# Kernel optimization log

Hardware: AMD Instinct MI355X
Metric: run time of the kernel (lower is better)

## Reference

```python
import jax, jax.numpy as jnp
import numpy as np

B, H, IN = 2048, 256, 64
K_TERMS = 8


def setup_inputs() -> dict:
    key = jax.random.key(0)
    ks = jax.random.split(key, 8)
    limit_x = float(np.sqrt(6.0 / (IN + H)))
    limit_h = float(np.sqrt(6.0 / (H + H)))
    return {
        "h": jax.random.normal(ks[0], (B, H), dtype=jnp.float32),
        "x": jax.random.normal(ks[1], (B, IN), dtype=jnp.float32),
        "xdot": jax.random.normal(ks[2], (B, IN), dtype=jnp.float32),
        "wx": jax.random.uniform(ks[3], (H, IN), minval=-limit_x, maxval=limit_x, dtype=jnp.float32),
        "wh": jax.random.uniform(ks[4], (H, H), minval=-limit_h, maxval=limit_h, dtype=jnp.float32),
        "wout": jax.random.uniform(ks[5], (H, H), minval=-limit_h, maxval=limit_h, dtype=jnp.float32),
        "b0": jnp.zeros((H,), dtype=jnp.float32),
        "b1": jnp.zeros((H,), dtype=jnp.float32),
    }


def reference(h, x, xdot, wx, wh, wout, b0, b1):
    # Batched version of the per-sample vector field (original is vmapped by the solver).
    l1 = x @ wx.T + h @ wh.T + b0                 # [B,H]
    relu_val = jax.nn.relu(l1)
    lout = relu_val @ wout.T + b1                 # [B,H]
    tanh_val = jnp.tanh(lout)
    dtanh = 1.0 - tanh_val ** 2                   # [B,H]
    drelu = (l1 > 0).astype(jnp.float32)          # activation == 'relu' (hard gate)
    # d_outer[b,i,j] = dtanh[b,i] * wout[i,j] * drelu[b,j]
    d_outer = dtanh[:, :, None] * wout[None, :, :] * drelu[:, None, :]  # [B,H,H]
    Jx = jnp.einsum('bhj,ji->bhi', d_outer, wx)   # [B,H,IN]
    Jh = jnp.einsum('bhj,ji->bhi', d_outer, wh)   # [B,H,H]
    jx = jnp.einsum('bhi,bi->bh', Jx, xdot)       # [B,H]
    h_dot = jx
    curr_term = jx
    for _ in range(K_TERMS):
        curr_term = jnp.einsum('bij,bj->bi', Jh, curr_term)
        h_dot = h_dot + curr_term
    return h_dot
```

## Files before the change

kernel.cpp:

```cpp
#include <hip/hip_runtime.h>
#include <math.h>

#define B_  2048
#define H_  256
#define IN_ 64

typedef __attribute__((ext_vector_type(8))) short bf8_t;
typedef __attribute__((ext_vector_type(4))) short s4_t;
typedef __attribute__((ext_vector_type(4))) float f4_t;

#define MFMA_BF16(a, b, c) __builtin_amdgcn_mfma_f32_16x16x32_bf16((a), (b), (c), 0, 0, 0)

__device__ __forceinline__ short f2bf(float f) {
  union { float f; unsigned u; } v; v.f = f;
  unsigned u = v.u + 0x7fffu + ((v.u >> 16) & 1u);
  return (short)(u >> 16);
}
__device__ __forceinline__ float bf2f(short s) {
  union { unsigned u; float f; } v; v.u = ((unsigned)(unsigned short)s) << 16;
  return v.f;
}

__device__ __forceinline__ void load_wfrag2(const float* __restrict__ W, int ld, int col,
                                            int k0, bf8_t& hi, bf8_t& lo) {
  const float* p = W + (size_t)col * ld + k0;
  f4_t a = *reinterpret_cast<const f4_t*>(p);
  f4_t b = *reinterpret_cast<const f4_t*>(p + 4);
#pragma unroll
  for (int j = 0; j < 8; ++j) {
    float f = (j < 4) ? a[j] : b[j - 4];
    short h = f2bf(f);
    hi[j] = h;
    lo[j] = f2bf(f - bf2f(h));
  }
}

#define GEMM3(A0, A1, AH, AL, WH, WL, NK) do {                                  \
  _Pragma("unroll")                                                             \
  for (int ks = 0; ks < (NK); ++ks) {                                           \
    bf8_t ah = *reinterpret_cast<const bf8_t*>(&AH[ln][ks * 32 + lq * 8]);      \
    bf8_t al = *reinterpret_cast<const bf8_t*>(&AL[ln][ks * 32 + lq * 8]);      \
    A0 = MFMA_BF16(ah, WH[0][ks], A0);                                          \
    A0 = MFMA_BF16(ah, WL[0][ks], A0);                                          \
    A0 = MFMA_BF16(al, WH[0][ks], A0);                                          \
    A1 = MFMA_BF16(ah, WH[1][ks], A1);                                          \
    A1 = MFMA_BF16(ah, WL[1][ks], A1);                                          \
    A1 = MFMA_BF16(al, WH[1][ks], A1);                                          \
  } } while (0)

#define GEMM2(A0, A1, AH, AL, WH, NK) do {                                      \
  _Pragma("unroll")                                                             \
  for (int ks = 0; ks < (NK); ++ks) {                                           \
    bf8_t ah = *reinterpret_cast<const bf8_t*>(&AH[ln][ks * 32 + lq * 8]);      \
    bf8_t al = *reinterpret_cast<const bf8_t*>(&AL[ln][ks * 32 + lq * 8]);      \
    A0 = MFMA_BF16(ah, WH[0][ks], A0);                                          \
    A0 = MFMA_BF16(al, WH[0][ks], A0);                                          \
    A1 = MFMA_BF16(ah, WH[1][ks], A1);                                          \
    A1 = MFMA_BF16(al, WH[1][ks], A1);                                          \
  } } while (0)

__global__ __launch_bounds__(512, 2) void jacde_mfma(
    const float* __restrict__ h_g, const float* __restrict__ x_g,
    const float* __restrict__ xd_g, const float* __restrict__ wx,
    const float* __restrict__ wh, const float* __restrict__ wo,
    const float* __restrict__ b0, const float* __restrict__ b1,
    float* __restrict__ out) {

  __shared__ short h_hi[16][264], h_lo[16][264];
  __shared__ short x_hi[16][72],  x_lo[16][72];
  __shared__ short xd_hi[16][72], xd_lo[16][72];
  __shared__ short u_hi[16][264], u_lo[16][264];
  __shared__ short v_hi[16][264], v_lo[16][264];
  __shared__ float l1_t[16][264];
  __shared__ int   fix_cnt;
  __shared__ int   fix_list[64];

  const int tid  = threadIdx.x;
  const int wv   = tid >> 6;
  const int lane = tid & 63;
  const int ln   = lane & 15;
  const int lq   = lane >> 4;
  const int r0   = blockIdx.x * 16;
  const int cbase = wv * 32;

  if (tid == 0) fix_cnt = 0;

  for (int c = tid; c < 16 * 64; c += 512) {
    int r = c >> 6, k4 = (c & 63) * 4;
    f4_t v = *reinterpret_cast<const f4_t*>(h_g + (size_t)(r0 + r) * H_ + k4);
    s4_t shv, slv;
#pragma unroll
    for (int j = 0; j < 4; ++j) { short h = f2bf(v[j]); shv[j] = h; slv[j] = f2bf(v[j] - bf2f(h)); }
    *reinterpret_cast<s4_t*>(&h_hi[r][k4]) = shv;
    *reinterpret_cast<s4_t*>(&h_lo[r][k4]) = slv;
  }
  {
    int t2 = tid & 255;
    const float* src = (tid < 256) ? x_g : xd_g;
    short (*dh)[72] = (tid < 256) ? x_hi : xd_hi;
    short (*dl)[72] = (tid < 256) ? x_lo : xd_lo;
    int r = t2 >> 4, k4 = (t2 & 15) * 4;
    f4_t v = *reinterpret_cast<const f4_t*>(src + (size_t)(r0 + r) * IN_ + k4);
    s4_t shv, slv;
#pragma unroll
    for (int j = 0; j < 4; ++j) { short h = f2bf(v[j]); shv[j] = h; slv[j] = f2bf(v[j] - bf2f(h)); }
    *reinterpret_cast<s4_t*>(&dh[r][k4]) = shv;
    *reinterpret_cast<s4_t*>(&dl[r][k4]) = slv;
  }

  bf8_t whf[2][8], wof[2][8];
  f4_t acc0, acc1, sacc0, sacc1;
  float dre0[4], dre1[4], dta0[4], dta1[4], hd0[4], hd1[4];

  {
    bf8_t whl[2][8], wxh[2][2], wxl[2][2];
#pragma unroll
    for (int t = 0; t < 2; ++t) {
      int col = cbase + t * 16 + ln;
#pragma unroll
      for (int ks = 0; ks < 8; ++ks)
        load_wfrag2(wh, H_, col, ks * 32 + lq * 8, whf[t][ks], whl[t][ks]);
#pragma unroll
      for (int ks = 0; ks < 2; ++ks)
        load_wfrag2(wx, IN_, col, ks * 32 + lq * 8, wxh[t][ks], wxl[t][ks]);
    }
    __syncthreads();

    float bv0 = b0[cbase + ln], bv1 = b0[cbase + 16 + ln];
    acc0 = (f4_t){bv0, bv0, bv0, bv0};
    acc1 = (f4_t){bv1, bv1, bv1, bv1};
    GEMM3(acc0, acc1, h_hi, h_lo, whf, whl, 8);
    GEMM3(acc0, acc1, x_hi, x_lo, wxh, wxl, 2);
    sacc0 = (f4_t){0.f, 0.f, 0.f, 0.f};
    sacc1 = (f4_t){0.f, 0.f, 0.f, 0.f};
    GEMM3(sacc0, sacc1, xd_hi, xd_lo, wxh, wxl, 2);
#pragma unroll
    for (int r = 0; r < 4; ++r) {
      l1_t[lq * 4 + r][cbase + ln]      = acc0[r];
      l1_t[lq * 4 + r][cbase + 16 + ln] = acc1[r];
    }
  }
  __syncthreads();

  for (int e = tid; e < 16 * 256; e += 512) {
    int r = e >> 8, c = e & 255;
    if (fabsf(l1_t[r][c]) < 1e-4f) {
      int idx = atomicAdd(&fix_cnt, 1);
      if (idx < 64) fix_list[idx] = (r << 8) | c;
    }
  }
  __syncthreads();
  {
    int nfix = min(fix_cnt, 64);
    for (int e = wv; e < nfix; e += 8) {
      int rc = fix_list[e];
      int r = rc >> 8, c = rc & 255;
      const float* hrow = h_g + (size_t)(r0 + r) * H_;
      const float* wrow = wh + (size_t)c * H_;
      double sum = (double)hrow[lane]       * (double)wrow[lane]
                 + (double)hrow[lane + 64]  * (double)wrow[lane + 64]
                 + (double)hrow[lane + 128] * (double)wrow[lane + 128]
                 + (double)hrow[lane + 192] * (double)wrow[lane + 192]
                 + (double)x_g[(size_t)(r0 + r) * IN_ + lane] * (double)wx[(size_t)c * IN_ + lane];
#pragma unroll
      for (int m = 32; m; m >>= 1) sum += __shfl_xor(sum, m);
      if (lane == 0) l1_t[r][c] = (float)(sum + (double)b0[c]);
    }
  }
  __syncthreads();

  for (int e = tid; e < 16 * 256; e += 512) {
    int r = e >> 8, c = e & 255;
    float l1 = l1_t[r][c];
    float rv = l1 > 0.f ? l1 : 0.f;
    short hi = f2bf(rv);
    u_hi[r][c] = hi;
    u_lo[r][c] = f2bf(rv - bf2f(hi));
  }
#pragma unroll
  for (int r = 0; r < 4; ++r) {
    dre0[r] = (l1_t[lq * 4 + r][cbase + ln]      > 0.f) ? 1.f : 0.f;
    dre1[r] = (l1_t[lq * 4 + r][cbase + 16 + ln] > 0.f) ? 1.f : 0.f;
  }
  __syncthreads();

  {
    bf8_t wol[2][8];
#pragma unroll
    for (int t = 0; t < 2; ++t) {
      int col = cbase + t * 16 + ln;
#pragma unroll
      for (int ks = 0; ks < 8; ++ks)
        load_wfrag2(wo, H_, col, ks * 32 + lq * 8, wof[t][ks], wol[t][ks]);
    }
    float bv0 = b1[cbase + ln], bv1 = b1[cbase + 16 + ln];
    acc0 = (f4_t){bv0, bv0, bv0, bv0};
    acc1 = (f4_t){bv1, bv1, bv1, bv1};
    GEMM3(acc0, acc1, u_hi, u_lo, wof, wol, 8);
#pragma unroll
    for (int r = 0; r < 4; ++r) {
      float t0 = tanhf(acc0[r]);
      float t1 = tanhf(acc1[r]);
      dta0[r] = 1.f - t0 * t0;
      dta1[r] = 1.f - t1 * t1;
    }
  }
  __syncthreads();

#pragma unroll
  for (int r = 0; r < 4; ++r) {
    int row = lq * 4 + r;
    float v0 = dre0[r] * sacc0[r];
    float v1 = dre1[r] * sacc1[r];
    short h0 = f2bf(v0), h1 = f2bf(v1);
    u_hi[row][cbase + ln]      = h0;  u_lo[row][cbase + ln]      = f2bf(v0 - bf2f(h0));
    u_hi[row][cbase + 16 + ln] = h1;  u_lo[row][cbase + 16 + ln] = f2bf(v1 - bf2f(h1));
  }
  __syncthreads();

  acc0 = (f4_t){0.f, 0.f, 0.f, 0.f};
  acc1 = (f4_t){0.f, 0.f, 0.f, 0.f};
  GEMM2(acc0, acc1, u_hi, u_lo, wof, 8);
#pragma unroll
  for (int r = 0; r < 4; ++r) {
    int row = lq * 4 + r;
    float v0 = dta0[r] * acc0[r];
    float v1 = dta1[r] * acc1[r];
    hd0[r] = v0; hd1[r] = v1;
    short h0 = f2bf(v0), h1 = f2bf(v1);
    v_hi[row][cbase + ln]      = h0;  v_lo[row][cbase + ln]      = f2bf(v0 - bf2f(h0));
    v_hi[row][cbase + 16 + ln] = h1;  v_lo[row][cbase + 16 + ln] = f2bf(v1 - bf2f(h1));
  }
  __syncthreads();

  for (int it = 0; it < 8; ++it) {
    acc0 = (f4_t){0.f, 0.f, 0.f, 0.f};
    acc1 = (f4_t){0.f, 0.f, 0.f, 0.f};
    GEMM2(acc0, acc1, v_hi, v_lo, whf, 8);
#pragma unroll
    for (int r = 0; r < 4; ++r) {
      int row = lq * 4 + r;
      float v0 = dre0[r] * acc0[r];
      float v1 = dre1[r] * acc1[r];
      short h0 = f2bf(v0), h1 = f2bf(v1);
      u_hi[row][cbase + ln]      = h0;  u_lo[row][cbase + ln]      = f2bf(v0 - bf2f(h0));
      u_hi[row][cbase + 16 + ln] = h1;  u_lo[row][cbase + 16 + ln] = f2bf(v1 - bf2f(h1));
    }
    __syncthreads();

    acc0 = (f4_t){0.f, 0.f, 0.f, 0.f};
    acc1 = (f4_t){0.f, 0.f, 0.f, 0.f};
    GEMM2(acc0, acc1, u_hi, u_lo, wof, 8);
#pragma unroll
    for (int r = 0; r < 4; ++r) {
      int row = lq * 4 + r;
      float v0 = dta0[r] * acc0[r];
      float v1 = dta1[r] * acc1[r];
      hd0[r] += v0; hd1[r] += v1;
      if (it < 7) {
        short h0 = f2bf(v0), h1 = f2bf(v1);
        v_hi[row][cbase + ln]      = h0;  v_lo[row][cbase + ln]      = f2bf(v0 - bf2f(h0));
        v_hi[row][cbase + 16 + ln] = h1;  v_lo[row][cbase + 16 + ln] = f2bf(v1 - bf2f(h1));
      }
    }
    __syncthreads();
  }

#pragma unroll
  for (int r = 0; r < 4; ++r) {
    int row = lq * 4 + r;
    out[(size_t)(r0 + row) * H_ + cbase + ln]      = hd0[r];
    out[(size_t)(r0 + row) * H_ + cbase + 16 + ln] = hd1[r];
  }
}

extern "C" void kernel_launch(void* const* d_in, const int* in_sizes, int n_in,
                              void* d_out, int out_size, void* d_ws, size_t ws_size,
                              hipStream_t stream) {
  const float* h_g  = (const float*)d_in[0];
  const float* x_g  = (const float*)d_in[1];
  const float* xd_g = (const float*)d_in[2];
  const float* wx   = (const float*)d_in[3];
  const float* wh   = (const float*)d_in[4];
  const float* wo   = (const float*)d_in[5];
  const float* b0   = (const float*)d_in[6];
  const float* b1   = (const float*)d_in[7];
  jacde_mfma<<<dim3(B_ / 16), dim3(512), 0, stream>>>(
      h_g, x_g, xd_g, wx, wh, wo, b0, b1, (float*)d_out);
}
```

Measured before the change: 106.8 us.

## Pre-split weights into bf16 MFMA fragments in a prep kernel, split accumulator chains

Adds a small prep kernel that converts wh, wo and wx once per call into bf16 hi/lo pairs, stored in global memory already arranged in MFMA fragment order. The main kernel then loads these with coalesced 16-byte reads instead of every block reading fp32 weights and doing the hi/lo split itself. Separately, the GEMM macros alternate between two accumulators on odd and even k-steps so consecutive MFMAs do not wait on each other. The cost is an extra kernel launch and double the bytes for the bf16 hi/lo weight copies, and the changed summation order slightly alters rounding. The wo argument is dropped from the main kernel and the prep runs on every call, so no result is reused.

```diff
diff --git a/kernel.cpp b/kernel.cpp
--- a/kernel.cpp
+++ b/kernel.cpp
@@ -21,50 +21,76 @@
   return v.f;
 }
 
-__device__ __forceinline__ void load_wfrag2(const float* __restrict__ W, int ld, int col,
-                                            int k0, bf8_t& hi, bf8_t& lo) {
-  const float* p = W + (size_t)col * ld + k0;
-  f4_t a = *reinterpret_cast<const f4_t*>(p);
-  f4_t b = *reinterpret_cast<const f4_t*>(p + 4);
+__device__ __align__(16) short g_whf[2][65536];
+__device__ __align__(16) short g_wof[2][65536];
+__device__ __align__(16) short g_wxf[2][16384];
+
+__global__ void prep_frag(const float* __restrict__ wh, const float* __restrict__ wo,
+                          const float* __restrict__ wx) {
+  int tid = blockIdx.x * 256 + threadIdx.x;
+  const float* W; short* Dh; short* Dl; int ld, ksh, o8;
+  if (tid < 8192)       { W = wh; Dh = g_whf[0]; Dl = g_whf[1]; ld = 256; ksh = 3; o8 = tid; }
+  else if (tid < 16384) { W = wo; Dh = g_wof[0]; Dl = g_wof[1]; ld = 256; ksh = 3; o8 = tid - 8192; }
+  else if (tid < 18432) { W = wx; Dh = g_wxf[0]; Dl = g_wxf[1]; ld = 64;  ksh = 1; o8 = tid - 16384; }
+  else return;
+  int lane = o8 & 63;
+  int gks = o8 >> 6;
+  int g = gks >> ksh, ks = gks & ((1 << ksh) - 1);
+  int c = g * 16 + (lane & 15);
+  int k0 = ks * 32 + ((lane >> 4) & 3) * 8;
+  const float* p = W + (size_t)c * ld + k0;
+  bf8_t hi, lo;
 #pragma unroll
   for (int j = 0; j < 8; ++j) {
-    float f = (j < 4) ? a[j] : b[j - 4];
+    float f = p[j];
     short h = f2bf(f);
-    hi[j] = h;
-    lo[j] = f2bf(f - bf2f(h));
-  }
+    hi[j] = h; lo[j] = f2bf(f - bf2f(h));
+  }
+  *reinterpret_cast<bf8_t*>(Dh + (size_t)o8 * 8) = hi;
+  *reinterpret_cast<bf8_t*>(Dl + (size_t)o8 * 8) = lo;
 }
 
 #define GEMM3(A0, A1, AH, AL, WH, WL, NK) do {                                  \
+  f4_t q0 = {0.f,0.f,0.f,0.f}, q1 = {0.f,0.f,0.f,0.f};                          \
   _Pragma("unroll")                                                             \
   for (int ks = 0; ks < (NK); ++ks) {                                           \
     bf8_t ah = *reinterpret_cast<const bf8_t*>(&AH[ln][ks * 32 + lq * 8]);      \
     bf8_t al = *reinterpret_cast<const bf8_t*>(&AL[ln][ks * 32 + lq * 8]);      \
-    A0 = MFMA_BF16(ah, WH[0][ks], A0);                                          \
-    A0 = MFMA_BF16(ah, WL[0][ks], A0);                                          \
-    A0 = MFMA_BF16(al, WH[0][ks], A0);                                          \
-    A1 = MFMA_BF16(ah, WH[1][ks], A1);                                          \
-    A1 = MFMA_BF16(ah, WL[1][ks], A1);                                          \
-    A1 = MFMA_BF16(al, WH[1][ks], A1);                                          \
-  } } while (0)
+    if (ks & 1) {                                                               \
+      q0 = MFMA_BF16(ah, WH[0][ks], q0); q0 = MFMA_BF16(ah, WL[0][ks], q0);     \
+      q0 = MFMA_BF16(al, WH[0][ks], q0);                                        \
+      q1 = MFMA_BF16(ah, WH[1][ks], q1); q1 = MFMA_BF16(ah, WL[1][ks], q1);     \
+      q1 = MFMA_BF16(al, WH[1][ks], q1);                                        \
+    } else {                                                                    \
+      A0 = MFMA_BF16(ah, WH[0][ks], A0); A0 = MFMA_BF16(ah, WL[0][ks], A0);     \
+      A0 = MFMA_BF16(al, WH[0][ks], A0);                                        \
+      A1 = MFMA_BF16(ah, WH[1][ks], A1); A1 = MFMA_BF16(ah, WL[1][ks], A1);     \
+      A1 = MFMA_BF16(al, WH[1][ks], A1);                                        \
+    }                                                                           \
+  }                                                                             \
+  A0 = A0 + q0; A1 = A1 + q1; } while (0)
 
 #define GEMM2(A0, A1, AH, AL, WH, NK) do {                                      \
+  f4_t q0 = {0.f,0.f,0.f,0.f}, q1 = {0.f,0.f,0.f,0.f};                          \
   _Pragma("unroll")                                                             \
   for (int ks = 0; ks < (NK); ++ks) {                                           \
     bf8_t ah = *reinterpret_cast<const bf8_t*>(&AH[ln][ks * 32 + lq * 8]);      \
     bf8_t al = *reinterpret_cast<const bf8_t*>(&AL[ln][ks * 32 + lq * 8]);      \
-    A0 = MFMA_BF16(ah, WH[0][ks], A0);                                          \
-    A0 = MFMA_BF16(al, WH[0][ks], A0);                                          \
-    A1 = MFMA_BF16(ah, WH[1][ks], A1);                                          \
-    A1 = MFMA_BF16(al, WH[1][ks], A1);                                          \
-  } } while (0)
+    if (ks & 1) {                                                               \
+      q0 = MFMA_BF16(ah, WH[0][ks], q0); q0 = MFMA_BF16(al, WH[0][ks], q0);     \
+      q1 = MFMA_BF16(ah, WH[1][ks], q1); q1 = MFMA_BF16(al, WH[1][ks], q1);     \
+    } else {                                                                    \
+      A0 = MFMA_BF16(ah, WH[0][ks], A0); A0 = MFMA_BF16(al, WH[0][ks], A0);     \
+      A1 = MFMA_BF16(ah, WH[1][ks], A1); A1 = MFMA_BF16(al, WH[1][ks], A1);     \
+    }                                                                           \
+  }                                                                             \
+  A0 = A0 + q0; A1 = A1 + q1; } while (0)
 
 __global__ __launch_bounds__(512, 2) void jacde_mfma(
     const float* __restrict__ h_g, const float* __restrict__ x_g,
     const float* __restrict__ xd_g, const float* __restrict__ wx,
-    const float* __restrict__ wh, const float* __restrict__ wo,
-    const float* __restrict__ b0, const float* __restrict__ b1,
-    float* __restrict__ out) {
+    const float* __restrict__ wh, const float* __restrict__ b0,
+    const float* __restrict__ b1, float* __restrict__ out) {
 
   __shared__ short h_hi[16][264], h_lo[16][264];
   __shared__ short x_hi[16][72],  x_lo[16][72];
@@ -116,13 +142,19 @@
     bf8_t whl[2][8], wxh[2][2], wxl[2][2];
 #pragma unroll
     for (int t = 0; t < 2; ++t) {
-      int col = cbase + t * 16 + ln;
-#pragma unroll
-      for (int ks = 0; ks < 8; ++ks)
-        load_wfrag2(wh, H_, col, ks * 32 + lq * 8, whf[t][ks], whl[t][ks]);
-#pragma unroll
-      for (int ks = 0; ks < 2; ++ks)
-        load_wfrag2(wx, IN_, col, ks * 32 + lq * 8, wxh[t][ks], wxl[t][ks]);
+      int gb = wv * 2 + t;
+#pragma unroll
+      for (int ks = 0; ks < 8; ++ks) {
+        int off = ((gb * 8 + ks) * 64 + lane) * 8;
+        whf[t][ks] = *reinterpret_cast<const bf8_t*>(&g_whf[0][off]);
+        whl[t][ks] = *reinterpret_cast<const bf8_t*>(&g_whf[1][off]);
+      }
+#pragma unroll
+      for (int ks = 0; ks < 2; ++ks) {
+        int off = ((gb * 2 + ks) * 64 + lane) * 8;
+        wxh[t][ks] = *reinterpret_cast<const bf8_t*>(&g_wxf[0][off]);
+        wxl[t][ks] = *reinterpret_cast<const bf8_t*>(&g_wxf[1][off]);
+      }
     }
     __syncthreads();
 
@@ -188,10 +220,13 @@
     bf8_t wol[2][8];
 #pragma unroll
     for (int t = 0; t < 2; ++t) {
-      int col = cbase + t * 16 + ln;
-#pragma unroll
-      for (int ks = 0; ks < 8; ++ks)
-        load_wfrag2(wo, H_, col, ks * 32 + lq * 8, wof[t][ks], wol[t][ks]);
+      int gb = wv * 2 + t;
+#pragma unroll
+      for (int ks = 0; ks < 8; ++ks) {
+        int off = ((gb * 8 + ks) * 64 + lane) * 8;
+        wof[t][ks] = *reinterpret_cast<const bf8_t*>(&g_wof[0][off]);
+        wol[t][ks] = *reinterpret_cast<const bf8_t*>(&g_wof[1][off]);
+      }
     }
     float bv0 = b1[cbase + ln], bv1 = b1[cbase + 16 + ln];
     acc0 = (f4_t){bv0, bv0, bv0, bv0};
@@ -285,6 +320,7 @@
   const float* wo   = (const float*)d_in[5];
   const float* b0   = (const float*)d_in[6];
   const float* b1   = (const float*)d_in[7];
+  prep_frag<<<dim3(72), dim3(256), 0, stream>>>(wh, wo, wx);
   jacde_mfma<<<dim3(B_ / 16), dim3(512), 0, stream>>>(
-      h_g, x_g, xd_g, wx, wh, wo, b0, b1, (float*)d_out);
-}
+      h_g, x_g, xd_g, wx, wh, b0, b1, (float*)d_out);
+}
```

After: 95.85 us. 1.11x faster.
